# Kernel optimization log

Hardware: AMD Instinct MI355X
Metric: run time of the kernel (lower is better)

## Reference

```python
import math
import jax, jax.numpy as jnp
import numpy as np

ANCHORS_SETTINGS = (
    dict(layer='p3', stride=32, size=48, scale=[2 ** (1.0 / 3.0), 2 ** (2.0 / 3.0)], aspect_ratio=[0.667, 1, 1.5]),
    dict(layer='p4', stride=64, size=96, scale=[2 ** (1.0 / 3.0), 2 ** (2.0 / 3.0)], aspect_ratio=[0.667, 1, 1.5]),
    dict(layer='p5', stride=128, size=192, scale=[1, 2 ** (1.0 / 3.0), 2 ** (2.0 / 3.0)], aspect_ratio=[0.667, 1, 1.5]),
)


def anchor_configs():
    # 21 static (kernel, stride, padding) configs, in the exact counter order of
    # weighted_anchor_aggregator (p3 x6, p4 x6, p5 x9).
    cfgs = []
    for info in ANCHORS_SETTINGS:
        stride, size = info['stride'], info['size']
        for scale in info['scale']:
            for ar in info['aspect_ratio']:
                kernel = (int(size * scale / float(ar) ** 0.5), int(size * scale * float(ar) ** 0.5))
                padding = (math.ceil((kernel[0] - stride) / 2.0), math.ceil((kernel[1] - stride) / 2.0))
                cfgs.append((kernel, (stride, stride), padding))
    return cfgs


def extract_weighted_patches(x, weights, kernel, stride, padding):
    # x: (B,H,W,C); weights: (B,k,gh,gw). Vectorized equivalent of the original
    # lax.scan over per-position dynamic_slice gathers:
    #   acc = sum_{i,j} weights[:,:,i,j] (x) x_pad[:, i*s : i*s+kh, j*s : j*s+kw, :]
    b = x.shape[0]
    _, k, gh, gw = weights.shape
    xp = jnp.pad(x, ((0, 0),
                     (padding[0], padding[0] + kernel[0]),
                     (padding[1], padding[1] + kernel[1]),
                     (0, 0)))
    rows = jnp.arange(gh)[:, None] * stride[0] + jnp.arange(kernel[0])[None, :]  # (gh, kh)
    cols = jnp.arange(gw)[:, None] * stride[1] + jnp.arange(kernel[1])[None, :]  # (gw, kw)
    # gather all strided patches: (B, gh, kh, gw, kw, C)
    patches = xp[:, rows][:, :, :, cols]
    # weighted sum over grid positions -> (B, k, kh, kw, C)
    return jnp.einsum('bkij,bihjwc->bkhwc', weights, patches)


def _aggregate(x, weights_p3, weights_p4, weights_p5):
    weights = ([weights_p3[:, a] for a in range(weights_p3.shape[1])]
               + [weights_p4[:, a] for a in range(weights_p4.shape[1])]
               + [weights_p5[:, a] for a in range(weights_p5.shape[1])])
    b, k = weights[0].shape[0], weights[0].shape[1]
    acc = jnp.zeros((b * k, 224, 224, 3), x.dtype)
    for w, (kernel, stride, padding) in zip(weights, anchor_configs()):
        agg = extract_weighted_patches(x, w, kernel, stride, padding)
        agg = agg.reshape(b * k, kernel[0], kernel[1], 3)
        acc = acc + jax.image.resize(agg, (b * k, 224, 224, 3), 'bilinear')
    return acc


def setup_inputs() -> dict:
    key = jax.random.key(0)
    k0, k1, k2, k3 = jax.random.split(key, 4)
    B, K = 8, 4
    return {
        'x': jax.random.normal(k0, (B, 448, 448, 3), jnp.float32),
        'weights_p3': jax.random.uniform(k1, (B, 6, K, 14, 14), jnp.float32),
        'weights_p4': jax.random.uniform(k2, (B, 6, K, 7, 7), jnp.float32),
        'weights_p5': jax.random.uniform(k3, (B, 9, K, 4, 4), jnp.float32),
    }


def reference(x, weights_p3, weights_p4, weights_p5):
    return _aggregate(x, weights_p3, weights_p4, weights_p5)
```

## Files before the change

### kernel.cpp

```cpp
#include <hip/hip_runtime.h>
#include <math.h>


#define BATCH 8
#define KK 4
#define OUT_HW 224
#define IMG_HW 448
#define NCFG 21

#define WTBL_BYTES (NCFG * 2 * OUT_HW * 16)
#define ITBL_BYTES (NCFG * 2 * OUT_HW * 4)
#define WT_OFF_BYTES (WTBL_BYTES + ITBL_BYTES)
#define WT_F4 12912
#define AGG_OFF_BYTES (WT_OFF_BYTES + WT_F4 * 16)

typedef float v2f __attribute__((ext_vector_type(2)));

static constexpr int cKH[NCFG]  = {74,60,49,93,76,62, 148,120,98,186,152,124,
                                   235,192,156,296,241,197,373,304,248};
static constexpr int cKW[NCFG]  = {49,60,74,62,76,93, 98,120,148,124,152,186,
                                   156,192,235,197,241,296,248,304,373};
static constexpr int cMTH[NCFG] = {2,2,2,2,2,2, 2,2,2,2,2,2, 3,2,2,3,3,2,4,3,3};
static constexpr int cMTW[NCFG] = {2,2,2,2,2,2, 2,2,2,2,2,2, 2,2,3,2,3,3,3,3,4};

__host__ __device__ constexpr int ckwp(int c) { return cKW[c] + (cKW[c] & 1); }
__host__ __device__ constexpr long cwsoff(int c, int g) {
    long o = 0;
    for (int k = g; k < c; ++k) o += (long)cKH[k] * ckwp(k) * (BATCH * KK);
    return o;
}

struct ACfg {
    int kh, kw, kwp, p0, p1;
    int layer;
    int ns;
    int wt_off;
    int ws_off;
    int block_start;
    int blocks_per_img;
};

struct AggArgs {
    ACfg e[NCFG];
    int n;
};

struct TablesArgs { int kh[NCFG]; int kw[NCFG]; };

struct TrArgs {
    int layer[NCFG];
    int anchor[NCFG];
    int gsz[NCFG];
    int wt_off[NCFG];
};

struct F3 { float a, b, c; };

__device__ inline unsigned int bf16_rne(float f) {
    unsigned int u = __float_as_uint(f);
    return (u + 0x7fffu + ((u >> 16) & 1u)) >> 16;
}

__global__ __launch_bounds__(256) void init_tables(float4* __restrict__ wtbl,
                                                   int* __restrict__ itbl,
                                                   TablesArgs t) {
    int cfg = blockIdx.x >> 1;
    int dim = blockIdx.x & 1;
    int o = threadIdx.x;
    if (o >= OUT_HW) return;
    int n = dim ? t.kw[cfg] : t.kh[cfg];

    float inv = (float)(1.0 / ((double)OUT_HW / (double)n));
    float ks  = inv > 1.f ? inv : 1.f;
    float rks = 1.f / ks;
    float sf  = ((float)o + 0.5f) * inv - 0.5f;
    int i0 = (int)ceilf(sf - ks);  if (i0 < 0) i0 = 0;
    int i1 = (int)floorf(sf + ks); if (i1 > n - 1) i1 = n - 1;
    float sum = 0.f;
    for (int i = i0; i <= i1; ++i) {
        float v = 1.f - fabsf((float)i - sf) * rks;
        sum += (v > 0.f ? v : 0.f);
    }
    float rsum = 1.f / sum;
    float w[4];
#pragma unroll
    for (int d = 0; d < 4; ++d) {
        int i = i0 + d;
        float v = 0.f;
        if (i <= i1) {
            v = 1.f - fabsf((float)i - sf) * rks;
            v = (v > 0.f ? v : 0.f) * rsum;
        }
        w[d] = v;
    }
    int idx = cfg * (2 * OUT_HW) + dim * OUT_HW + o;
    wtbl[idx] = make_float4(w[0], w[1], w[2], w[3]);
    itbl[idx] = i0;
}

__global__ __launch_bounds__(256) void transpose_w(
        const float* __restrict__ wp3, const float* __restrict__ wp4,
        const float* __restrict__ wp5, float4* __restrict__ wT, TrArgs t) {
    int cfg = blockIdx.x;
    int b = blockIdx.y;
    int gsz = t.gsz[cfg];
    const float* base;
    int A;
    if (t.layer[cfg] == 0)      { base = wp3; A = 6; }
    else if (t.layer[cfg] == 1) { base = wp4; A = 6; }
    else                        { base = wp5; A = 9; }
    const float* src = base + (size_t)(b * A + t.anchor[cfg]) * (KK * gsz);
    for (int g = threadIdx.x; g < gsz; g += 256) {
        wT[t.wt_off[cfg] + b * gsz + g] =
            make_float4(src[0 * gsz + g], src[1 * gsz + g],
                        src[2 * gsz + g], src[3 * gsz + g]);
    }
}

template <int GH, int GW, int STRIDE, int L2S>
__device__ inline void agg_body(const ACfg& c, int b, int h, int slot,
                                const float* __restrict__ xb,
                                const float4* __restrict__ wlds,
                                uint2* __restrict__ agg) {
    const int w0 = (((slot >> L2S) << (L2S + 1)) | (slot & (STRIDE - 1)));
    const int w1 = w0 + STRIDE;
    const bool two = w1 < c.kw;

    v2f acc2[4][3];
#pragma unroll
    for (int k = 0; k < 4; ++k)
#pragma unroll
        for (int ch = 0; ch < 3; ++ch) { acc2[k][ch].x = 0.f; acc2[k][ch].y = 0.f; }

    const int rb = h - c.p0;
    int ilo = rb >= 0 ? 0 : (-rb + STRIDE - 1) / STRIDE;
    int ihi = (IMG_HW - 1 - rb) / STRIDE;
    if (ihi > GH - 1) ihi = GH - 1;

    const int cb = w0 - c.p1;

    int  cof[GW + 1];
    bool ok [GW + 1];
#pragma unroll
    for (int jj = 0; jj <= GW; ++jj) {
        int col = cb + jj * STRIDE;
        ok[jj] = (unsigned)col < (unsigned)IMG_HW;
        unsigned cc = (unsigned)col;
        if (cc > (unsigned)(IMG_HW - 1)) cc = (unsigned)(IMG_HW - 1);
        cof[jj] = (int)cc * 3;
    }

#pragma unroll 1
    for (int i = ilo; i <= ihi; ++i) {
        const float* xr = xb + (size_t)(rb + i * STRIDE) * (IMG_HW * 3);
        const float4* wrow = wlds + i * GW;

        float px[GW + 1][3];
#pragma unroll
        for (int jj = 0; jj <= GW; ++jj) {
            F3 v = *(const F3*)(xr + cof[jj]);
            px[jj][0] = ok[jj] ? v.a : 0.f;
            px[jj][1] = ok[jj] ? v.b : 0.f;
            px[jj][2] = ok[jj] ? v.c : 0.f;
        }

#pragma unroll
        for (int j = 0; j < GW; ++j) {
            float4 wk = wrow[j];
            v2f d0 = {px[j][0], px[j + 1][0]};
            v2f d1 = {px[j][1], px[j + 1][1]};
            v2f d2 = {px[j][2], px[j + 1][2]};
            v2f wv0 = {wk.x, wk.x};
            v2f wv1 = {wk.y, wk.y};
            v2f wv2 = {wk.z, wk.z};
            v2f wv3 = {wk.w, wk.w};
            acc2[0][0] = __builtin_elementwise_fma(wv0, d0, acc2[0][0]);
            acc2[0][1] = __builtin_elementwise_fma(wv0, d1, acc2[0][1]);
            acc2[0][2] = __builtin_elementwise_fma(wv0, d2, acc2[0][2]);
            acc2[1][0] = __builtin_elementwise_fma(wv1, d0, acc2[1][0]);
            acc2[1][1] = __builtin_elementwise_fma(wv1, d1, acc2[1][1]);
            acc2[1][2] = __builtin_elementwise_fma(wv1, d2, acc2[1][2]);
            acc2[2][0] = __builtin_elementwise_fma(wv2, d0, acc2[2][0]);
            acc2[2][1] = __builtin_elementwise_fma(wv2, d1, acc2[2][1]);
            acc2[2][2] = __builtin_elementwise_fma(wv2, d2, acc2[2][2]);
            acc2[3][0] = __builtin_elementwise_fma(wv3, d0, acc2[3][0]);
            acc2[3][1] = __builtin_elementwise_fma(wv3, d1, acc2[3][1]);
            acc2[3][2] = __builtin_elementwise_fma(wv3, d2, acc2[3][2]);
        }
    }

    const int npix = c.kh * c.kwp;
#pragma unroll
    for (int k = 0; k < 4; ++k) {
        size_t base = (size_t)c.ws_off + (size_t)(b * KK + k) * npix
                    + (size_t)h * c.kwp + w0;
        uint2 o0;
        o0.x = bf16_rne(acc2[k][0].x) | (bf16_rne(acc2[k][1].x) << 16);
        o0.y = bf16_rne(acc2[k][2].x);
        agg[base] = o0;
        if (two) {
            uint2 o1;
            o1.x = bf16_rne(acc2[k][0].y) | (bf16_rne(acc2[k][1].y) << 16);
            o1.y = bf16_rne(acc2[k][2].y);
            agg[base + STRIDE] = o1;
        }
    }
}

__global__ __launch_bounds__(256, 3) void agg_all(
        const float* __restrict__ x,
        const float4* __restrict__ wT,
        uint2* __restrict__ agg,
        AggArgs a) {
    int bid = blockIdx.x;
    int ci = 0;
    while (ci + 1 < a.n && bid >= a.e[ci + 1].block_start) ci++;
    const ACfg c = a.e[ci];
    int local = bid - c.block_start;
    int b     = local & 7;
    int sblk  = local >> 3;

    const int gsz = (c.layer == 0) ? 196 : (c.layer == 1) ? 49 : 16;
    __shared__ float4 wlds[196];
    for (int t = threadIdx.x; t < gsz; t += 256)
        wlds[t] = wT[c.wt_off + b * gsz + t];
    __syncthreads();

    int pidx = sblk * 256 + (int)threadIdx.x;
    if (pidx >= c.kh * c.ns) return;
    int h    = pidx / c.ns;
    int slot = pidx - h * c.ns;

    const float* __restrict__ xb = x + (size_t)b * (IMG_HW * IMG_HW * 3);
    if (c.layer == 0)      agg_body<14, 14, 32, 5>(c, b, h, slot, xb, wlds, agg);
    else if (c.layer == 1) agg_body<7, 7, 64, 6>(c, b, h, slot, xb, wlds, agg);
    else                   agg_body<4, 4, 128, 7>(c, b, h, slot, xb, wlds, agg);
}

template <int TH, int TW, int KH_, int KW_, int KWP_>
__device__ inline void taps_ct(const uint2* __restrict__ base,
                               int i0, int j0,
                               float4 wh4, float4 ww4,
                               float& a0, float& a1, float& a2) {
    const float* wh = (const float*)&wh4;
    const float* ww = (const float*)&ww4;
    uint2 v[TH][TW];
#pragma unroll
    for (int d = 0; d < TH; ++d) {
        int gi = i0 + d;
        if (gi > KH_ - 1) gi = KH_ - 1;
        const uint2* rp = base + (size_t)gi * KWP_;
#pragma unroll
        for (int e = 0; e < TW; ++e) {
            int gj = j0 + e;
            if (gj > KW_ - 1) gj = KW_ - 1;
            v[d][e] = rp[gj];
        }
    }
#pragma unroll
    for (int d = 0; d < TH; ++d) {
        float r0 = 0.f, r1 = 0.f, r2 = 0.f;
#pragma unroll
        for (int e = 0; e < TW; ++e) {
            uint2 t = v[d][e];
            float c0 = __uint_as_float(t.x << 16);
            float c1 = __uint_as_float(t.x & 0xffff0000u);
            float c2 = __uint_as_float(t.y << 16);
            float w = ww[e];
            r0 = fmaf(w, c0, r0);
            r1 = fmaf(w, c1, r1);
            r2 = fmaf(w, c2, r2);
        }
        a0 = fmaf(wh[d], r0, a0);
        a1 = fmaf(wh[d], r1, a1);
        a2 = fmaf(wh[d], r2, a2);
    }
}

template <int C, int CEND, int CSTART>
__device__ inline void do_rounds(const uint2* __restrict__ agg,
                                 const float4* __restrict__ wlds,
                                 const int* __restrict__ ilds,
                                 int bk, int tx, int ty,
                                 float& a0, float& a1, float& a2) {
    if constexpr (C < CEND) {
        constexpr int li  = C - CSTART;
        constexpr int kh  = cKH[C];
        constexpr int kw  = cKW[C];
        constexpr int kwp = ckwp(C);
        constexpr long wso = cwsoff(C, CSTART);
        float4 wh4 = wlds[li * 32 + ty];
        float4 ww4 = wlds[li * 32 + 16 + tx];
        int i0 = ilds[li * 32 + ty];
        int j0 = ilds[li * 32 + 16 + tx];
        const uint2* plane = agg + wso + (size_t)bk * (kh * kwp);
        taps_ct<cMTH[C], cMTW[C], kh, kw, kwp>(plane, i0, j0, wh4, ww4,
                                               a0, a1, a2);
        do_rounds<C + 1, CEND, CSTART>(agg, wlds, ilds, bk, tx, ty,
                                       a0, a1, a2);
    }
}

template <int CSTART, int CEND>
__global__ __launch_bounds__(256, 4) void resize_static(
        const uint2* __restrict__ agg,
        const float4* __restrict__ wtbl,
        const int* __restrict__ itbl,
        float* __restrict__ out,
        int accumulate) {
    constexpr int NC = CEND - CSTART;
    const int tid = threadIdx.x;
    const int tx = tid & 15;
    const int ty = tid >> 4;
    const int xo = blockIdx.x * 16 + tx;
    const int yo = blockIdx.y * 16 + ty;
    const int bk = blockIdx.z;

    __shared__ float4 wlds[NC * 32];
    __shared__ int    ilds[NC * 32];

    for (int e = tid; e < NC * 32; e += 256) {
        int ci  = e >> 5;
        int r   = e & 31;
        int isW = r >> 4;
        int idx = r & 15;
        int base_o = isW ? (blockIdx.x * 16) : (blockIdx.y * 16);
        int src = (CSTART + ci) * (2 * OUT_HW) + isW * OUT_HW + base_o + idx;
        wlds[ci * 32 + r] = wtbl[src];
        ilds[ci * 32 + r] = itbl[src];
    }
    __syncthreads();

    size_t ob = (((size_t)bk * OUT_HW + yo) * OUT_HW + xo) * 3;
    float a0, a1, a2;
    if (accumulate) {
        a0 = out[ob]; a1 = out[ob + 1]; a2 = out[ob + 2];
    } else {
        a0 = a1 = a2 = 0.f;
    }

    do_rounds<CSTART, CEND, CSTART>(agg, wlds, ilds, bk, tx, ty, a0, a1, a2);

    out[ob + 0] = a0; out[ob + 1] = a1; out[ob + 2] = a2;
}

extern "C" void kernel_launch(void* const* d_in, const int* in_sizes, int n_in,
                              void* d_out, int out_size, void* d_ws, size_t ws_size,
                              hipStream_t stream) {
    const float* x   = (const float*)d_in[0];
    const float* wp3 = (const float*)d_in[1];
    const float* wp4 = (const float*)d_in[2];
    const float* wp5 = (const float*)d_in[3];
    float* out = (float*)d_out;
    float4* wtbl = (float4*)d_ws;
    int*    itbl = (int*)((char*)d_ws + WTBL_BYTES);
    float4* wT   = (float4*)((char*)d_ws + WT_OFF_BYTES);
    uint2*  agg  = (uint2*)((char*)d_ws + AGG_OFF_BYTES);

    struct { int stride, size, nscale; double scales[3]; int gh; } layers[3] = {
        {32, 48, 2, {pow(2.0, 1.0 / 3.0), pow(2.0, 2.0 / 3.0), 0.0}, 14},
        {64, 96, 2, {pow(2.0, 1.0 / 3.0), pow(2.0, 2.0 / 3.0), 0.0}, 7},
        {128, 192, 3, {1.0, pow(2.0, 1.0 / 3.0), pow(2.0, 2.0 / 3.0)}, 4},
    };
    const double ars[3] = {0.667, 1.0, 1.5};

    struct HostCfg {
        int kh, kw, kwp, stride, p0, p1, gh, gw, layer, anchor, wt_off;
        int ns, blocks_per_img;
    } cfg[NCFG];
    TablesArgs ta;
    TrArgs tr;
    int nc = 0, wt_run = 0;
    for (int L = 0; L < 3; ++L) {
        int anchor = 0;
        for (int si = 0; si < layers[L].nscale; ++si) {
            for (int ai = 0; ai < 3; ++ai) {
                double ss = (double)layers[L].size * layers[L].scales[si];
                double sq = pow(ars[ai], 0.5);
                int kh = (int)(ss / sq);
                int kw = (int)(ss * sq);
                HostCfg& e = cfg[nc];
                e.kh = kh; e.kw = kw;
                e.kwp = kw + (kw & 1);
                e.stride = layers[L].stride;
                e.p0 = (int)ceil((double)(kh - layers[L].stride) / 2.0);
                e.p1 = (int)ceil((double)(kw - layers[L].stride) / 2.0);
                e.gh = layers[L].gh; e.gw = layers[L].gh;
                e.layer = L; e.anchor = anchor++;
                int s = e.stride;
                int q = kw / s, r = kw % s;
                e.ns = ((q + 1) / 2) * s + ((q % 2 == 0) ? r : 0);
                e.blocks_per_img = (kh * e.ns + 255) / 256;
                e.wt_off = wt_run;
                int gsz = e.gh * e.gw;
                wt_run += BATCH * gsz;
                ta.kh[nc] = kh; ta.kw[nc] = kw;
                tr.layer[nc] = L; tr.anchor[nc] = e.anchor;
                tr.gsz[nc] = gsz; tr.wt_off[nc] = e.wt_off;
                ++nc;
            }
        }
    }

    init_tables<<<NCFG * 2, 256, 0, stream>>>(wtbl, itbl, ta);
    transpose_w<<<dim3(NCFG, BATCH), 256, 0, stream>>>(wp3, wp4, wp5, wT, tr);

    dim3 rgrid(OUT_HW / 16, OUT_HW / 16, BATCH * KK);

    auto build = [&](int gstart, int gend, AggArgs& aa) -> int {
        aa.n = 0;
        int ablocks = 0;
        size_t off = 0;
        for (int c = gstart; c < gend; ++c) {
            ACfg& lc = aa.e[aa.n++];
            lc.kh = cfg[c].kh; lc.kw = cfg[c].kw; lc.kwp = cfg[c].kwp;
            lc.p0 = cfg[c].p0; lc.p1 = cfg[c].p1;
            lc.layer = cfg[c].layer;
            lc.ns = cfg[c].ns;
            lc.wt_off = cfg[c].wt_off;
            lc.ws_off = (int)off;
            lc.block_start = ablocks;
            lc.blocks_per_img = cfg[c].blocks_per_img;
            ablocks += cfg[c].blocks_per_img * BATCH;
            off += (size_t)cfg[c].kh * cfg[c].kwp * (BATCH * KK);
        }
        return ablocks;
    };

    AggArgs aa;
    int nb;

    nb = build(0, 15, aa);
    agg_all<<<nb, 256, 0, stream>>>(x, wT, agg, aa);
    resize_static<0, 15><<<rgrid, 256, 0, stream>>>(agg, wtbl, itbl, out, 0);

    nb = build(15, 19, aa);
    agg_all<<<nb, 256, 0, stream>>>(x, wT, agg, aa);
    resize_static<15, 19><<<rgrid, 256, 0, stream>>>(agg, wtbl, itbl, out, 1);

    nb = build(19, 21, aa);
    agg_all<<<nb, 256, 0, stream>>>(x, wT, agg, aa);
    resize_static<19, 21><<<rgrid, 256, 0, stream>>>(agg, wtbl, itbl, out, 1);

    (void)in_sizes; (void)n_in; (void)out_size; (void)ws_size;
}
```

Before: 271.9 us.

## Interleave K planes in bf16 agg buffer and resize two K per thread

Changes the intermediate aggregate buffer layout from per-(b,k) planes to pixel-major with the four K values interleaved, so the aggregation kernel writes 16-byte vector stores and the resize kernel reads two K values per 16-byte load. Each resize thread now computes two output images (k pair) using packed v2f FMAs, halving the grid z dimension. This cuts gather instruction count and index arithmetic per output but doubles per-thread register state and halves the number of resize blocks.

After: 266.0 us. 1.02x faster.

```diff
diff --git a/kernel.cpp b/kernel.cpp
--- a/kernel.cpp
+++ b/kernel.cpp
@@ -190,20 +190,34 @@
     }
 
     const int npix = c.kh * c.kwp;
-#pragma unroll
-    for (int k = 0; k < 4; ++k) {
-        size_t base = (size_t)c.ws_off + (size_t)(b * KK + k) * npix
-                    + (size_t)h * c.kwp + w0;
-        uint2 o0;
-        o0.x = bf16_rne(acc2[k][0].x) | (bf16_rne(acc2[k][1].x) << 16);
-        o0.y = bf16_rne(acc2[k][2].x);
-        agg[base] = o0;
-        if (two) {
-            uint2 o1;
-            o1.x = bf16_rne(acc2[k][0].y) | (bf16_rne(acc2[k][1].y) << 16);
-            o1.y = bf16_rne(acc2[k][2].y);
-            agg[base + STRIDE] = o1;
-        }
+    size_t pb0 = (size_t)c.ws_off
+               + ((size_t)b * npix + (size_t)h * c.kwp + w0) * KK;
+    {
+        uint4 s0, s1;
+        s0.x = bf16_rne(acc2[0][0].x) | (bf16_rne(acc2[0][1].x) << 16);
+        s0.y = bf16_rne(acc2[0][2].x);
+        s0.z = bf16_rne(acc2[1][0].x) | (bf16_rne(acc2[1][1].x) << 16);
+        s0.w = bf16_rne(acc2[1][2].x);
+        s1.x = bf16_rne(acc2[2][0].x) | (bf16_rne(acc2[2][1].x) << 16);
+        s1.y = bf16_rne(acc2[2][2].x);
+        s1.z = bf16_rne(acc2[3][0].x) | (bf16_rne(acc2[3][1].x) << 16);
+        s1.w = bf16_rne(acc2[3][2].x);
+        *(uint4*)(agg + pb0)     = s0;
+        *(uint4*)(agg + pb0 + 2) = s1;
+    }
+    if (two) {
+        size_t pb1 = pb0 + (size_t)STRIDE * KK;
+        uint4 s0, s1;
+        s0.x = bf16_rne(acc2[0][0].y) | (bf16_rne(acc2[0][1].y) << 16);
+        s0.y = bf16_rne(acc2[0][2].y);
+        s0.z = bf16_rne(acc2[1][0].y) | (bf16_rne(acc2[1][1].y) << 16);
+        s0.w = bf16_rne(acc2[1][2].y);
+        s1.x = bf16_rne(acc2[2][0].y) | (bf16_rne(acc2[2][1].y) << 16);
+        s1.y = bf16_rne(acc2[2][2].y);
+        s1.z = bf16_rne(acc2[3][0].y) | (bf16_rne(acc2[3][1].y) << 16);
+        s1.w = bf16_rne(acc2[3][2].y);
+        *(uint4*)(agg + pb1)     = s0;
+        *(uint4*)(agg + pb1 + 2) = s1;
     }
 }
 
@@ -238,42 +252,47 @@
 }
 
 template <int TH, int TW, int KH_, int KW_, int KWP_>
-__device__ inline void taps_ct(const uint2* __restrict__ base,
-                               int i0, int j0,
-                               float4 wh4, float4 ww4,
-                               float& a0, float& a1, float& a2) {
+__device__ inline void taps_ct2(const uint2* __restrict__ pb,
+                                int i0, int j0,
+                                float4 wh4, float4 ww4,
+                                v2f (&a)[3]) {
     const float* wh = (const float*)&wh4;
     const float* ww = (const float*)&ww4;
-    uint2 v[TH][TW];
+    uint4 v[TH][TW];
 #pragma unroll
     for (int d = 0; d < TH; ++d) {
         int gi = i0 + d;
         if (gi > KH_ - 1) gi = KH_ - 1;
-        const uint2* rp = base + (size_t)gi * KWP_;
+        const uint2* rp = pb + (size_t)gi * (KWP_ * KK);
 #pragma unroll
         for (int e = 0; e < TW; ++e) {
             int gj = j0 + e;
             if (gj > KW_ - 1) gj = KW_ - 1;
-            v[d][e] = rp[gj];
+            v[d][e] = *(const uint4*)(rp + gj * KK);
         }
     }
 #pragma unroll
     for (int d = 0; d < TH; ++d) {
-        float r0 = 0.f, r1 = 0.f, r2 = 0.f;
+        v2f r0 = {0.f, 0.f}, r1 = {0.f, 0.f}, r2 = {0.f, 0.f};
 #pragma unroll
         for (int e = 0; e < TW; ++e) {
-            uint2 t = v[d][e];
-            float c0 = __uint_as_float(t.x << 16);
-            float c1 = __uint_as_float(t.x & 0xffff0000u);
-            float c2 = __uint_as_float(t.y << 16);
-            float w = ww[e];
-            r0 = fmaf(w, c0, r0);
-            r1 = fmaf(w, c1, r1);
-            r2 = fmaf(w, c2, r2);
-        }
-        a0 = fmaf(wh[d], r0, a0);
-        a1 = fmaf(wh[d], r1, a1);
-        a2 = fmaf(wh[d], r2, a2);
+            uint4 q = v[d][e];
+            v2f c0, c1, c2;
+            c0.x = __uint_as_float(q.x << 16);
+            c0.y = __uint_as_float(q.z << 16);
+            c1.x = __uint_as_float(q.x & 0xffff0000u);
+            c1.y = __uint_as_float(q.z & 0xffff0000u);
+            c2.x = __uint_as_float(q.y << 16);
+            c2.y = __uint_as_float(q.w << 16);
+            v2f w2 = {ww[e], ww[e]};
+            r0 = __builtin_elementwise_fma(w2, c0, r0);
+            r1 = __builtin_elementwise_fma(w2, c1, r1);
+            r2 = __builtin_elementwise_fma(w2, c2, r2);
+        }
+        v2f h2 = {wh[d], wh[d]};
+        a[0] = __builtin_elementwise_fma(h2, r0, a[0]);
+        a[1] = __builtin_elementwise_fma(h2, r1, a[1]);
+        a[2] = __builtin_elementwise_fma(h2, r2, a[2]);
     }
 }
 
@@ -281,8 +300,8 @@
 __device__ inline void do_rounds(const uint2* __restrict__ agg,
                                  const float4* __restrict__ wlds,
                                  const int* __restrict__ ilds,
-                                 int bk, int tx, int ty,
-                                 float& a0, float& a1, float& a2) {
+                                 int b, int kp, int tx, int ty,
+                                 v2f (&a)[3]) {
     if constexpr (C < CEND) {
         constexpr int li  = C - CSTART;
         constexpr int kh  = cKH[C];
@@ -293,11 +312,10 @@
         float4 ww4 = wlds[li * 32 + 16 + tx];
         int i0 = ilds[li * 32 + ty];
         int j0 = ilds[li * 32 + 16 + tx];
-        const uint2* plane = agg + wso + (size_t)bk * (kh * kwp);
-        taps_ct<cMTH[C], cMTW[C], kh, kw, kwp>(plane, i0, j0, wh4, ww4,
-                                               a0, a1, a2);
-        do_rounds<C + 1, CEND, CSTART>(agg, wlds, ilds, bk, tx, ty,
-                                       a0, a1, a2);
+        const uint2* pb = agg + wso
+                        + (size_t)b * ((size_t)kh * kwp * KK) + kp * 2;
+        taps_ct2<cMTH[C], cMTW[C], kh, kw, kwp>(pb, i0, j0, wh4, ww4, a);
+        do_rounds<C + 1, CEND, CSTART>(agg, wlds, ilds, b, kp, tx, ty, a);
     }
 }
 
@@ -314,7 +332,8 @@
     const int ty = tid >> 4;
     const int xo = blockIdx.x * 16 + tx;
     const int yo = blockIdx.y * 16 + ty;
-    const int bk = blockIdx.z;
+    const int b  = blockIdx.z >> 1;
+    const int kp = blockIdx.z & 1;
 
     __shared__ float4 wlds[NC * 32];
     __shared__ int    ilds[NC * 32];
@@ -331,17 +350,22 @@
     }
     __syncthreads();
 
-    size_t ob = (((size_t)bk * OUT_HW + yo) * OUT_HW + xo) * 3;
-    float a0, a1, a2;
+    size_t obA = ((((size_t)(b * KK + kp * 2)) * OUT_HW + yo) * OUT_HW + xo) * 3;
+    size_t obB = obA + (size_t)OUT_HW * OUT_HW * 3;
+
+    v2f a[3];
     if (accumulate) {
-        a0 = out[ob]; a1 = out[ob + 1]; a2 = out[ob + 2];
+        a[0].x = out[obA + 0]; a[0].y = out[obB + 0];
+        a[1].x = out[obA + 1]; a[1].y = out[obB + 1];
+        a[2].x = out[obA + 2]; a[2].y = out[obB + 2];
     } else {
-        a0 = a1 = a2 = 0.f;
-    }
-
-    do_rounds<CSTART, CEND, CSTART>(agg, wlds, ilds, bk, tx, ty, a0, a1, a2);
-
-    out[ob + 0] = a0; out[ob + 1] = a1; out[ob + 2] = a2;
+        a[0] = v2f{0.f, 0.f}; a[1] = v2f{0.f, 0.f}; a[2] = v2f{0.f, 0.f};
+    }
+
+    do_rounds<CSTART, CEND, CSTART>(agg, wlds, ilds, b, kp, tx, ty, a);
+
+    out[obA + 0] = a[0].x; out[obA + 1] = a[1].x; out[obA + 2] = a[2].x;
+    out[obB + 0] = a[0].y; out[obB + 1] = a[1].y; out[obB + 2] = a[2].y;
 }
 
 extern "C" void kernel_launch(void* const* d_in, const int* in_sizes, int n_in,
@@ -405,7 +429,7 @@
     init_tables<<<NCFG * 2, 256, 0, stream>>>(wtbl, itbl, ta);
     transpose_w<<<dim3(NCFG, BATCH), 256, 0, stream>>>(wp3, wp4, wp5, wT, tr);
 
-    dim3 rgrid(OUT_HW / 16, OUT_HW / 16, BATCH * KK);
+    dim3 rgrid(OUT_HW / 16, OUT_HW / 16, BATCH * 2);
 
     auto build = [&](int gstart, int gend, AggArgs& aa) -> int {
         aa.n = 0;
```
